# Performance work log

Measured on AMD Instinct MI355X. Metric: run time of the kernel, lower is better.

## Reference

```python
import math
import jax, jax.numpy as jnp
import numpy as np

N, DIM, HIDDEN, E, K = 131072, 256, 512, 16, 2
TEMP = 1.0
CAP_F = 1.1
CAPACITY = max(1, math.ceil(N * K / float(E) * CAP_F))  # static, = 18023


def setup_inputs() -> dict:
    key = jax.random.key(0)
    ks = jax.random.split(key, 4)
    s_in = 1.0 / math.sqrt(DIM)
    s_h = 1.0 / math.sqrt(HIDDEN)
    return {
        "context": jax.random.normal(ks[0], (N, DIM), jnp.float32),
        "Wg": jax.random.uniform(ks[1], (DIM, E), jnp.float32, -s_in, s_in),
        "bg": jnp.zeros((E,), jnp.float32),
        "W1": jax.random.uniform(ks[2], (E, DIM, HIDDEN), jnp.float32, -s_in, s_in),
        "b1": jnp.zeros((E, HIDDEN), jnp.float32),
        "W2": jax.random.uniform(ks[3], (E, HIDDEN, DIM), jnp.float32, -s_h, s_h),
        "b2": jnp.zeros((E, DIM), jnp.float32),
    }


def reference(context, Wg, bg, W1, b1, W2, b2):
    # ---- router ----
    logits = context @ Wg + bg                    # [N, E]
    scaled = logits / TEMP
    probs = jax.nn.softmax(scaled, axis=-1)
    top_vals, top_idx = jax.lax.top_k(scaled, K)  # [N, K], sorted desc like torch.topk
    gate_scores = jax.nn.softmax(top_vals, axis=-1)

    # ---- capacity-padded dispatch (replicates per-expert topk-by-score drop) ----
    S = N * K
    assign = top_idx.reshape(-1)                  # [S] expert id per slot
    score = gate_scores.reshape(-1)               # [S]
    token = jnp.arange(S, dtype=jnp.int32) // K   # [S] source token per slot

    # group slots by expert, descending gate score within each expert
    order = jnp.lexsort((-score, assign))         # primary key: assign; secondary: -score
    a_s = assign[order]
    s_s = score[order]
    t_s = token[order]

    counts = jnp.bincount(assign, length=E)                       # [E]
    starts = jnp.concatenate([jnp.zeros((1,), counts.dtype), jnp.cumsum(counts)[:-1]])
    rank = jnp.arange(S) - starts[a_s]                            # rank within expert
    slot = jnp.where(rank < CAPACITY, rank, CAPACITY)             # OOB slots get dropped

    tok_tab = jnp.zeros((E, CAPACITY), jnp.int32).at[a_s, slot].set(t_s, mode="drop")
    sc_tab = jnp.zeros((E, CAPACITY), context.dtype).at[a_s, slot].set(s_s, mode="drop")
    valid = jnp.zeros((E, CAPACITY), context.dtype).at[a_s, slot].set(1.0, mode="drop")

    # ---- grouped expert MLP on gathered tokens ----
    x = context[tok_tab]                                          # [E, C, dim]
    h = jax.nn.relu(jnp.einsum('ecd,edh->ech', x, W1) + b1[:, None, :])
    y = jnp.einsum('ech,ehd->ecd', h, W2) + b2[:, None, :]        # [E, C, dim]
    y = y * (sc_tab * valid)[..., None]

    # ---- combine (scatter-add back to tokens) ----
    output = jnp.zeros_like(context).at[tok_tab.reshape(-1)].add(y.reshape(-1, DIM))

    # ---- aux stats ----
    dispatch = valid.sum(axis=1)                                  # [E]
    load = dispatch / jnp.maximum(dispatch.sum(), 1.0)
    importance = probs.mean(axis=0)
    aux_loss = (importance * load).sum() * E
    entropy = -(probs * jnp.log(jnp.maximum(probs, 1e-9))).sum(axis=-1).mean()
    return output, aux_loss, entropy, dispatch
```

## Files before the change

### kernel.cpp

```cpp
#include <hip/hip_runtime.h>
#include <hip/hip_bf16.h>
#include <math.h>

#define N_TOK 131072
#define DIM 256
#define HID 512
#define NE 16
#define CAP 18023

typedef __bf16 bf16_t;
typedef __bf16 bf16x4 __attribute__((ext_vector_type(4)));
typedef __bf16 bf16x8 __attribute__((ext_vector_type(8)));
typedef float floatx4 __attribute__((ext_vector_type(4)));

#define OFF_CNT 0
#define OFF_IMP 1024
#define OFF_ENT 2048
#define OFF_TOK 4096
#define OFF_SC 1157568
#define OFF_W1T 2311168
#define OFF_W2T 6505472

__global__ void k_zero(float* __restrict__ out, int* __restrict__ cnt,
                       float* __restrict__ imp, float* __restrict__ ent) {
  const int nthreads = 2048 * 256;
  int tid = blockIdx.x * 256 + threadIdx.x;
  float4* o4 = (float4*)out;
  float4 z = make_float4(0.f, 0.f, 0.f, 0.f);
#pragma unroll
  for (int j = 0; j < 16; j++) o4[(size_t)j * nthreads + tid] = z;
  if (blockIdx.x == 0) {
    if (threadIdx.x < NE) { cnt[threadIdx.x * 16] = 0; imp[threadIdx.x * 16] = 0.f; }
    if (threadIdx.x == NE) ent[0] = 0.f;
  }
}

__global__ void k_transpose(const float* __restrict__ src, bf16_t* __restrict__ dst,
                            int R, int C) {
  __shared__ float tile[32][33];
  int e = blockIdx.z;
  int c0 = blockIdx.x * 32;
  int r0 = blockIdx.y * 32;
  const float* s = src + (size_t)e * R * C;
  bf16_t* d = dst + (size_t)e * R * C;
  int tx = threadIdx.x, ty = threadIdx.y;
#pragma unroll
  for (int i = 0; i < 4; i++)
    tile[ty + i * 8][tx] = s[(size_t)(r0 + ty + i * 8) * C + (c0 + tx)];
  __syncthreads();
#pragma unroll
  for (int i = 0; i < 4; i++)
    d[(size_t)(c0 + ty + i * 8) * R + (r0 + tx)] = (bf16_t)tile[tx][ty + i * 8];
}

__launch_bounds__(256, 2)
__global__ void k_router(const float* __restrict__ ctx, const float* __restrict__ Wg,
                         const float* __restrict__ bg, int* __restrict__ cnt,
                         int* __restrict__ tok_list, float* __restrict__ sc_list,
                         float* __restrict__ imp, float* __restrict__ ent) {
  __shared__ double wg64[DIM * NE];
  __shared__ float xt[256 * 33];
  __shared__ int lcnt[NE];
  __shared__ int lbase[NE];
  __shared__ float limp[NE];
  __shared__ float lent;
  const int tid = threadIdx.x;
  const int tok0 = blockIdx.x * 256;

  for (int i = 0; i < 16; i++) {
    int idx = i * 256 + tid;
    wg64[idx] = (double)Wg[idx];
  }
  if (tid < NE) { lcnt[tid] = 0; limp[tid] = 0.f; }
  if (tid == NE) lent = 0.f;

  double acc[NE];
#pragma unroll
  for (int e = 0; e < NE; e++) acc[e] = (double)bg[e];

  for (int c = 0; c < 8; c++) {
    __syncthreads();
    const float* src = ctx + (size_t)tok0 * DIM + c * 32;
#pragma unroll
    for (int i = 0; i < 8; i++) {
      int f = i * 256 + tid;
      int row = f >> 3;
      int c4 = f & 7;
      float4 v = *(const float4*)(src + (size_t)row * DIM + c4 * 4);
      float* dstp = &xt[row * 33 + c4 * 4];
      dstp[0] = v.x; dstp[1] = v.y; dstp[2] = v.z; dstp[3] = v.w;
    }
    __syncthreads();
#pragma unroll
    for (int d = 0; d < 32; d++) {
      double x = (double)xt[tid * 33 + d];
      const double* wrow = &wg64[(c * 32 + d) * NE];
#pragma unroll
      for (int e = 0; e < NE; e++) acc[e] = fma(x, wrow[e], acc[e]);
    }
  }

  double v1 = -1e300, v2 = -1e300;
  int i1 = 0, i2 = 0;
#pragma unroll
  for (int e = 0; e < NE; e++) {
    double v = acc[e];
    if (v > v1) { v2 = v1; i2 = i1; v1 = v; i1 = e; }
    else if (v > v2) { v2 = v; i2 = e; }
  }

  float p[NE];
  float s = 0.f;
#pragma unroll
  for (int e = 0; e < NE; e++) { p[e] = expf((float)(acc[e] - v1)); s += p[e]; }
  float inv = 1.f / s;
  float entl = 0.f;
#pragma unroll
  for (int e = 0; e < NE; e++) {
    float pe = p[e] * inv; p[e] = pe;
    entl -= pe * logf(fmaxf(pe, 1e-9f));
  }

  double rr = exp(v2 - v1);
  double den = 1.0 + rr;
  float g1 = (float)(1.0 / den);
  float g2 = (float)(rr / den);

  int p1 = atomicAdd(&lcnt[i1], 1);
  int p2 = atomicAdd(&lcnt[i2], 1);
  __syncthreads();
  if (tid < NE) lbase[tid] = atomicAdd(&cnt[tid * 16], lcnt[tid]);
  __syncthreads();

  int token = tok0 + tid;
  int pos = lbase[i1] + p1;
  if (pos < CAP) { tok_list[i1 * CAP + pos] = token; sc_list[i1 * CAP + pos] = g1; }
  pos = lbase[i2] + p2;
  if (pos < CAP) { tok_list[i2 * CAP + pos] = token; sc_list[i2 * CAP + pos] = g2; }

#pragma unroll
  for (int e = 0; e < NE; e++) {
    float v = p[e];
#pragma unroll
    for (int o = 32; o > 0; o >>= 1) v += __shfl_down(v, o);
    if ((tid & 63) == 0) atomicAdd(&limp[e], v);
  }
  {
    float v = entl;
#pragma unroll
    for (int o = 32; o > 0; o >>= 1) v += __shfl_down(v, o);
    if ((tid & 63) == 0) atomicAdd(&lent, v);
  }
  __syncthreads();
  if (tid < NE) atomicAdd(&imp[tid * 16], limp[tid]);
  if (tid == NE) atomicAdd(ent, lent);
}

#define XB_STRIDE 264
#define HB_STRIDE 520

__launch_bounds__(256, 2)
__global__ void k_expert(const float* __restrict__ ctx,
                         const bf16_t* __restrict__ W1T, const float* __restrict__ b1,
                         const bf16_t* __restrict__ W2T, const float* __restrict__ b2,
                         const int* __restrict__ cnt,
                         const int* __restrict__ tok_list, const float* __restrict__ sc_list,
                         float* __restrict__ out) {
  __shared__ __align__(16) char smem_raw[64 * HB_STRIDE * 2];
  __shared__ int tok_s[64];
  __shared__ float sc_s[64];
  __shared__ float b1s[HID];
  __shared__ float b2s[DIM];
  bf16_t* xb = (bf16_t*)smem_raw;
  bf16_t* hb = (bf16_t*)smem_raw;

  const int bid = blockIdx.x;
  const int e = (bid & 7) * 2 + ((bid >> 3) & 1);
  const int chunk = bid >> 4;

  const int count = min(cnt[e * 16], CAP);
  const int m0 = chunk * 64;
  if (m0 >= count) return;
  const int rem = min(64, count - m0);

  const int tid = threadIdx.x;
  const int lane = tid & 63;
  const int w = tid >> 6;
  const int L15 = lane & 15;
  const int quad = lane >> 4;

  if (tid < 64) {
    int t = 0; float sgate = 0.f;
    if (tid < rem) {
      t = tok_list[e * CAP + m0 + tid];
      sgate = sc_list[e * CAP + m0 + tid];
    }
    tok_s[tid] = t; sc_s[tid] = sgate;
  }
  for (int i = tid; i < HID; i += 256) b1s[i] = b1[e * HID + i];
  for (int i = tid; i < DIM; i += 256) b2s[i] = b2[e * DIM + i];
  __syncthreads();

#pragma unroll
  for (int i = 0; i < 16; i++) {
    int f = i * 256 + tid;
    int row = f >> 6;
    int c4 = f & 63;
    float4 v = *(const float4*)(ctx + (size_t)tok_s[row] * DIM + c4 * 4);
    bf16x4 bv;
    bv[0] = (bf16_t)v.x; bv[1] = (bf16_t)v.y; bv[2] = (bf16_t)v.z; bv[3] = (bf16_t)v.w;
    *(bf16x4*)(xb + row * XB_STRIDE + c4 * 4) = bv;
  }
  __syncthreads();

  floatx4 acc1[8][4];
#pragma unroll
  for (int it = 0; it < 8; it++)
#pragma unroll
    for (int jt = 0; jt < 4; jt++) {
      floatx4 z = {0.f, 0.f, 0.f, 0.f};
      acc1[it][jt] = z;
    }

  const bf16_t* w1e = W1T + (size_t)e * HID * DIM;
#pragma unroll
  for (int k = 0; k < 8; k++) {
    bf16x8 afr[8];
#pragma unroll
    for (int it = 0; it < 8; it++) {
      int n = w * 128 + it * 16 + L15;
      afr[it] = *(const bf16x8*)(w1e + n * DIM + k * 32 + quad * 8);
    }
    bf16x8 bfr[4];
#pragma unroll
    for (int jt = 0; jt < 4; jt++) {
      int m = jt * 16 + L15;
      bfr[jt] = *(const bf16x8*)(xb + m * XB_STRIDE + k * 32 + quad * 8);
    }
#pragma unroll
    for (int it = 0; it < 8; it++)
#pragma unroll
      for (int jt = 0; jt < 4; jt++)
        acc1[it][jt] = __builtin_amdgcn_mfma_f32_16x16x32_bf16(afr[it], bfr[jt],
                                                               acc1[it][jt], 0, 0, 0);
  }
  __syncthreads();

#pragma unroll
  for (int it = 0; it < 8; it++) {
    int n0 = w * 128 + it * 16 + quad * 4;
    float4 bb = *(const float4*)(&b1s[n0]);
#pragma unroll
    for (int jt = 0; jt < 4; jt++) {
      int m = jt * 16 + L15;
      bf16x4 hv;
      hv[0] = (bf16_t)fmaxf(acc1[it][jt][0] + bb.x, 0.f);
      hv[1] = (bf16_t)fmaxf(acc1[it][jt][1] + bb.y, 0.f);
      hv[2] = (bf16_t)fmaxf(acc1[it][jt][2] + bb.z, 0.f);
      hv[3] = (bf16_t)fmaxf(acc1[it][jt][3] + bb.w, 0.f);
      *(bf16x4*)(hb + m * HB_STRIDE + n0) = hv;
    }
  }
  __syncthreads();

  floatx4 acc2[4][4];
#pragma unroll
  for (int mt = 0; mt < 4; mt++)
#pragma unroll
    for (int dt = 0; dt < 4; dt++) {
      floatx4 z = {0.f, 0.f, 0.f, 0.f};
      acc2[mt][dt] = z;
    }

  const bf16_t* w2e = W2T + (size_t)e * DIM * HID;
#pragma unroll
  for (int k = 0; k < 16; k++) {
    bf16x8 afr[4];
#pragma unroll
    for (int mt = 0; mt < 4; mt++)
      afr[mt] = *(const bf16x8*)(hb + (mt * 16 + L15) * HB_STRIDE + k * 32 + quad * 8);
    bf16x8 bfr[4];
#pragma unroll
    for (int dt = 0; dt < 4; dt++) {
      int d = w * 64 + dt * 16 + L15;
      bfr[dt] = *(const bf16x8*)(w2e + d * HID + k * 32 + quad * 8);
    }
#pragma unroll
    for (int mt = 0; mt < 4; mt++)
#pragma unroll
      for (int dt = 0; dt < 4; dt++)
        acc2[mt][dt] = __builtin_amdgcn_mfma_f32_16x16x32_bf16(afr[mt], bfr[dt],
                                                               acc2[mt][dt], 0, 0, 0);
  }

#pragma unroll
  for (int mt = 0; mt < 4; mt++) {
#pragma unroll
    for (int r = 0; r < 4; r++) {
      int m = mt * 16 + quad * 4 + r;
      int t = tok_s[m];
      float sg = sc_s[m];
      float* orow = out + (size_t)t * DIM;
#pragma unroll
      for (int dt = 0; dt < 4; dt++) {
        int d = w * 64 + dt * 16 + L15;
        float v = (acc2[mt][dt][r] + b2s[d]) * sg;
        atomicAdd(orow + d, v);
      }
    }
  }
}

__global__ void k_finalize(const int* __restrict__ cnt, const float* __restrict__ imp,
                           const float* __restrict__ ent, float* __restrict__ out) {
  if (threadIdx.x == 0 && blockIdx.x == 0) {
    double tot = 0.0;
    float disp[NE];
    for (int e = 0; e < NE; e++) {
      int c = min(cnt[e * 16], CAP);
      disp[e] = (float)c;
      tot += (double)c;
    }
    double denom = tot > 0.0 ? tot : 1.0;
    double aux = 0.0;
    for (int e = 0; e < NE; e++)
      aux += ((double)imp[e * 16] / (double)N_TOK) * ((double)disp[e] / denom);
    float* tail = out + (size_t)N_TOK * DIM;
    tail[0] = (float)(aux * (double)NE);
    tail[1] = (float)((double)ent[0] / (double)N_TOK);
    for (int e = 0; e < NE; e++) tail[2 + e] = disp[e];
  }
}

extern "C" void kernel_launch(void* const* d_in, const int* in_sizes, int n_in,
                              void* d_out, int out_size, void* d_ws, size_t ws_size,
                              hipStream_t stream) {
  const float* ctx = (const float*)d_in[0];
  const float* Wg = (const float*)d_in[1];
  const float* bg = (const float*)d_in[2];
  const float* W1 = (const float*)d_in[3];
  const float* b1 = (const float*)d_in[4];
  const float* W2 = (const float*)d_in[5];
  const float* b2 = (const float*)d_in[6];
  float* out = (float*)d_out;
  char* ws = (char*)d_ws;

  int* cnt = (int*)(ws + OFF_CNT);
  float* imp = (float*)(ws + OFF_IMP);
  float* ent = (float*)(ws + OFF_ENT);
  int* tok_list = (int*)(ws + OFF_TOK);
  float* sc_list = (float*)(ws + OFF_SC);
  bf16_t* W1T = (bf16_t*)(ws + OFF_W1T);
  bf16_t* W2T = (bf16_t*)(ws + OFF_W2T);

  k_zero<<<2048, 256, 0, stream>>>(out, cnt, imp, ent);
  k_transpose<<<dim3(HID / 32, DIM / 32, NE), dim3(32, 8), 0, stream>>>(W1, W1T, DIM, HID);
  k_transpose<<<dim3(DIM / 32, HID / 32, NE), dim3(32, 8), 0, stream>>>(W2, W2T, HID, DIM);
  k_router<<<N_TOK / 256, 256, 0, stream>>>(ctx, Wg, bg, cnt, tok_list, sc_list, imp, ent);
  k_expert<<<4512, 256, 0, stream>>>(ctx, W1T, b1, W2T, b2, cnt, tok_list, sc_list, out);
  k_finalize<<<1, 64, 0, stream>>>(cnt, imp, ent, out);
}
```

Baseline: 701.7 us.

## Replace atomic scatter-add combine with bf16 expert buffer and gather kernel

The expert kernel now writes gate-scaled outputs as bf16 into a per-expert slot buffer, and a new combine kernel gathers each token's two slots through an inverse index recorded by the router. This removes the fp32 atomicAdd scatter into the output and the full zeroing pass over the output. The router's fp64 weight reads from shared memory are also vectorized into 4-wide loads. The gather path is used only when the workspace is large enough, and rounding outputs to bf16 before summing adds some precision loss.

```diff
diff --git a/kernel.cpp b/kernel.cpp
--- a/kernel.cpp
+++ b/kernel.cpp
@@ -12,6 +12,7 @@
 typedef __bf16 bf16x4 __attribute__((ext_vector_type(4)));
 typedef __bf16 bf16x8 __attribute__((ext_vector_type(8)));
 typedef float floatx4 __attribute__((ext_vector_type(4)));
+typedef double doublex4 __attribute__((ext_vector_type(4)));
 
 #define OFF_CNT 0
 #define OFF_IMP 1024
@@ -20,19 +21,23 @@
 #define OFF_SC 1157568
 #define OFF_W1T 2311168
 #define OFF_W2T 6505472
-
-__global__ void k_zero(float* __restrict__ out, int* __restrict__ cnt,
-                       float* __restrict__ imp, float* __restrict__ ent) {
+#define OFF_INV 10699776
+#define OFF_Y 11748352
+#define WS_NEED (11748352UL + (size_t)NE * CAP * DIM * 2)
+
+__global__ void k_init(int* __restrict__ cnt, float* __restrict__ imp,
+                       float* __restrict__ ent) {
+  if (threadIdx.x < NE) { cnt[threadIdx.x * 16] = 0; imp[threadIdx.x * 16] = 0.f; }
+  if (threadIdx.x == NE) ent[0] = 0.f;
+}
+
+__global__ void k_zero_out(float* __restrict__ out) {
   const int nthreads = 2048 * 256;
   int tid = blockIdx.x * 256 + threadIdx.x;
   float4* o4 = (float4*)out;
   float4 z = make_float4(0.f, 0.f, 0.f, 0.f);
 #pragma unroll
   for (int j = 0; j < 16; j++) o4[(size_t)j * nthreads + tid] = z;
-  if (blockIdx.x == 0) {
-    if (threadIdx.x < NE) { cnt[threadIdx.x * 16] = 0; imp[threadIdx.x * 16] = 0.f; }
-    if (threadIdx.x == NE) ent[0] = 0.f;
-  }
 }
 
 __global__ void k_transpose(const float* __restrict__ src, bf16_t* __restrict__ dst,
@@ -57,8 +62,9 @@
 __global__ void k_router(const float* __restrict__ ctx, const float* __restrict__ Wg,
                          const float* __restrict__ bg, int* __restrict__ cnt,
                          int* __restrict__ tok_list, float* __restrict__ sc_list,
+                         int* __restrict__ inv,
                          float* __restrict__ imp, float* __restrict__ ent) {
-  __shared__ double wg64[DIM * NE];
+  __shared__ __align__(32) double wg64[DIM * NE];
   __shared__ float xt[256 * 33];
   __shared__ int lcnt[NE];
   __shared__ int lbase[NE];
@@ -96,7 +102,13 @@
       double x = (double)xt[tid * 33 + d];
       const double* wrow = &wg64[(c * 32 + d) * NE];
 #pragma unroll
-      for (int e = 0; e < NE; e++) acc[e] = fma(x, wrow[e], acc[e]);
+      for (int ee = 0; ee < 4; ee++) {
+        doublex4 wv = *(const doublex4*)(wrow + ee * 4);
+        acc[ee * 4 + 0] = fma(x, wv[0], acc[ee * 4 + 0]);
+        acc[ee * 4 + 1] = fma(x, wv[1], acc[ee * 4 + 1]);
+        acc[ee * 4 + 2] = fma(x, wv[2], acc[ee * 4 + 2]);
+        acc[ee * 4 + 3] = fma(x, wv[3], acc[ee * 4 + 3]);
+      }
     }
   }
 
@@ -113,11 +125,11 @@
   float s = 0.f;
 #pragma unroll
   for (int e = 0; e < NE; e++) { p[e] = expf((float)(acc[e] - v1)); s += p[e]; }
-  float inv = 1.f / s;
+  float inv_s = 1.f / s;
   float entl = 0.f;
 #pragma unroll
   for (int e = 0; e < NE; e++) {
-    float pe = p[e] * inv; p[e] = pe;
+    float pe = p[e] * inv_s; p[e] = pe;
     entl -= pe * logf(fmaxf(pe, 1e-9f));
   }
 
@@ -134,9 +146,13 @@
 
   int token = tok0 + tid;
   int pos = lbase[i1] + p1;
-  if (pos < CAP) { tok_list[i1 * CAP + pos] = token; sc_list[i1 * CAP + pos] = g1; }
+  int l1 = -1;
+  if (pos < CAP) { tok_list[i1 * CAP + pos] = token; sc_list[i1 * CAP + pos] = g1; l1 = i1 * CAP + pos; }
   pos = lbase[i2] + p2;
-  if (pos < CAP) { tok_list[i2 * CAP + pos] = token; sc_list[i2 * CAP + pos] = g2; }
+  int l2 = -1;
+  if (pos < CAP) { tok_list[i2 * CAP + pos] = token; sc_list[i2 * CAP + pos] = g2; l2 = i2 * CAP + pos; }
+  inv[token * 2] = l1;
+  inv[token * 2 + 1] = l2;
 
 #pragma unroll
   for (int e = 0; e < NE; e++) {
@@ -159,13 +175,14 @@
 #define XB_STRIDE 264
 #define HB_STRIDE 520
 
+template <bool GATHER>
 __launch_bounds__(256, 2)
 __global__ void k_expert(const float* __restrict__ ctx,
                          const bf16_t* __restrict__ W1T, const float* __restrict__ b1,
                          const bf16_t* __restrict__ W2T, const float* __restrict__ b2,
                          const int* __restrict__ cnt,
                          const int* __restrict__ tok_list, const float* __restrict__ sc_list,
-                         float* __restrict__ out) {
+                         bf16_t* __restrict__ y_buf, float* __restrict__ out) {
   __shared__ __align__(16) char smem_raw[64 * HB_STRIDE * 2];
   __shared__ int tok_s[64];
   __shared__ float sc_s[64];
@@ -173,6 +190,7 @@
   __shared__ float b2s[DIM];
   bf16_t* xb = (bf16_t*)smem_raw;
   bf16_t* hb = (bf16_t*)smem_raw;
+  bf16_t* yb = (bf16_t*)smem_raw;
 
   const int bid = blockIdx.x;
   const int e = (bid & 7) * 2 + ((bid >> 3) & 1);
@@ -293,21 +311,75 @@
                                                                acc2[mt][dt], 0, 0, 0);
   }
 
-#pragma unroll
-  for (int mt = 0; mt < 4; mt++) {
-#pragma unroll
-    for (int r = 0; r < 4; r++) {
-      int m = mt * 16 + quad * 4 + r;
-      int t = tok_s[m];
-      float sg = sc_s[m];
-      float* orow = out + (size_t)t * DIM;
-#pragma unroll
-      for (int dt = 0; dt < 4; dt++) {
-        int d = w * 64 + dt * 16 + L15;
-        float v = (acc2[mt][dt][r] + b2s[d]) * sg;
-        atomicAdd(orow + d, v);
+  if (GATHER) {
+    __syncthreads();
+#pragma unroll
+    for (int mt = 0; mt < 4; mt++) {
+#pragma unroll
+      for (int r = 0; r < 4; r++) {
+        int m = mt * 16 + quad * 4 + r;
+        float sg = sc_s[m];
+#pragma unroll
+        for (int dt = 0; dt < 4; dt++) {
+          int d = w * 64 + dt * 16 + L15;
+          yb[m * XB_STRIDE + d] = (bf16_t)((acc2[mt][dt][r] + b2s[d]) * sg);
+        }
       }
     }
+    __syncthreads();
+    bf16_t* ybase = y_buf + ((size_t)e * CAP + m0) * DIM;
+#pragma unroll
+    for (int i = 0; i < 16; i++) {
+      int row = i * 4 + w;
+      if (row < rem) {
+        bf16x4 v = *(const bf16x4*)(yb + row * XB_STRIDE + lane * 4);
+        *(bf16x4*)(ybase + (size_t)row * DIM + lane * 4) = v;
+      }
+    }
+  } else {
+#pragma unroll
+    for (int mt = 0; mt < 4; mt++) {
+#pragma unroll
+      for (int r = 0; r < 4; r++) {
+        int m = mt * 16 + quad * 4 + r;
+        int t = tok_s[m];
+        float sg = sc_s[m];
+        float* orow = out + (size_t)t * DIM;
+#pragma unroll
+        for (int dt = 0; dt < 4; dt++) {
+          int d = w * 64 + dt * 16 + L15;
+          float v = (acc2[mt][dt][r] + b2s[d]) * sg;
+          atomicAdd(orow + d, v);
+        }
+      }
+    }
+  }
+}
+
+__global__ void k_combine(const bf16_t* __restrict__ y_buf, const int* __restrict__ inv,
+                          float* __restrict__ out) {
+  __shared__ int loc_s[128];
+  const int tid = threadIdx.x;
+  const int tok0 = blockIdx.x * 64;
+  if (tid < 128) loc_s[tid] = inv[tok0 * 2 + tid];
+  __syncthreads();
+  const int w = tid >> 6;
+  const int lane = tid & 63;
+#pragma unroll
+  for (int i = 0; i < 16; i++) {
+    int row = i * 4 + w;
+    int l1 = loc_s[row * 2];
+    int l2 = loc_s[row * 2 + 1];
+    float4 o = make_float4(0.f, 0.f, 0.f, 0.f);
+    if (l1 >= 0) {
+      bf16x4 a = *(const bf16x4*)(y_buf + (size_t)l1 * DIM + lane * 4);
+      o.x += (float)a[0]; o.y += (float)a[1]; o.z += (float)a[2]; o.w += (float)a[3];
+    }
+    if (l2 >= 0) {
+      bf16x4 b = *(const bf16x4*)(y_buf + (size_t)l2 * DIM + lane * 4);
+      o.x += (float)b[0]; o.y += (float)b[1]; o.z += (float)b[2]; o.w += (float)b[3];
+    }
+    *(float4*)(out + (size_t)(tok0 + row) * DIM + lane * 4) = o;
   }
 }
 
@@ -352,11 +424,23 @@
   float* sc_list = (float*)(ws + OFF_SC);
   bf16_t* W1T = (bf16_t*)(ws + OFF_W1T);
   bf16_t* W2T = (bf16_t*)(ws + OFF_W2T);
-
-  k_zero<<<2048, 256, 0, stream>>>(out, cnt, imp, ent);
+  int* inv = (int*)(ws + OFF_INV);
+  bf16_t* y_buf = (bf16_t*)(ws + OFF_Y);
+
+  const bool gather = ws_size >= WS_NEED;
+
+  k_init<<<1, 64, 0, stream>>>(cnt, imp, ent);
+  if (!gather) k_zero_out<<<2048, 256, 0, stream>>>(out);
   k_transpose<<<dim3(HID / 32, DIM / 32, NE), dim3(32, 8), 0, stream>>>(W1, W1T, DIM, HID);
   k_transpose<<<dim3(DIM / 32, HID / 32, NE), dim3(32, 8), 0, stream>>>(W2, W2T, HID, DIM);
-  k_router<<<N_TOK / 256, 256, 0, stream>>>(ctx, Wg, bg, cnt, tok_list, sc_list, imp, ent);
-  k_expert<<<4512, 256, 0, stream>>>(ctx, W1T, b1, W2T, b2, cnt, tok_list, sc_list, out);
+  k_router<<<N_TOK / 256, 256, 0, stream>>>(ctx, Wg, bg, cnt, tok_list, sc_list, inv, imp, ent);
+  if (gather) {
+    k_expert<true><<<4512, 256, 0, stream>>>(ctx, W1T, b1, W2T, b2, cnt, tok_list, sc_list,
+                                             y_buf, out);
+    k_combine<<<N_TOK / 64, 256, 0, stream>>>(y_buf, inv, out);
+  } else {
+    k_expert<false><<<4512, 256, 0, stream>>>(ctx, W1T, b1, W2T, b2, cnt, tok_list, sc_list,
+                                              y_buf, out);
+  }
   k_finalize<<<1, 64, 0, stream>>>(cnt, imp, ent, out);
 }
```

Result: faster. 627.3 us (-10.6%).
